# Performance work log

Measured on AMD Instinct MI355X. Metric: run time of the kernel, lower is better.

Reference implementation:

```python
import jax, jax.numpy as jnp
import numpy as np

B, N, TOKEN_DIM = 8, 1024, 768
H, D = 12, 64  # n_heads, head_dim


def setup_inputs() -> dict:
    key = jax.random.key(0)
    k1, k2, k3, k4 = jax.random.split(key, 4)
    x = jax.random.normal(k1, (B, N, TOKEN_DIM), dtype=jnp.float32)
    # nn.Linear(token_dim, 3*H*D, bias=False); store as (in, out)
    W_qkv = jax.random.normal(k2, (TOKEN_DIM, 3 * H * D), dtype=jnp.float32) * (TOKEN_DIM ** -0.5)
    # nn.Linear(H*D, token_dim) with bias
    W_out = jax.random.normal(k3, (H * D, TOKEN_DIM), dtype=jnp.float32) * ((H * D) ** -0.5)
    b_out = jax.random.normal(k4, (TOKEN_DIM,), dtype=jnp.float32) * 0.01
    return {"x": x, "W_qkv": W_qkv, "W_out": W_out, "b_out": b_out}


def reference(x, W_qkv, W_out, b_out):
    b, n, _ = x.shape
    qkv = x @ W_qkv                              # (B, N, 3*H*D)
    # Faithful to original: reshape directly to (B, 3, H, N, D)
    qkv = qkv.reshape(b, 3, H, n, D)
    q, k, v = qkv[:, 0], qkv[:, 1], qkv[:, 2]    # each (B, H, N, D)
    scale = D ** -0.5
    scores = jnp.einsum('bhnd,bhmd->bhnm', q, k) * scale
    probs = jax.nn.softmax(scores, axis=-1)
    attn = jnp.einsum('bhnm,bhmd->bhnd', probs, v)  # (B, H, N, D)
    attn = attn.transpose(0, 2, 1, 3).reshape(b, n, H * D)
    out = attn @ W_out + b_out                    # dropout p=0.0 is identity
    return out
```

## Files before the change

kernel.cpp:

```cpp
#include <hip/hip_runtime.h>
#include <math.h>

static constexpr int NB   = 8;
static constexpr int SEQ  = 1024;
static constexpr int TD   = 768;
static constexpr int NH   = 12;
static constexpr int HD   = 64;
static constexpr int QKVC = 3 * NH * HD;

static constexpr size_t BATCH_ELEMS = (size_t)SEQ * QKVC;
static constexpr size_t THIRD_ELEMS = (size_t)NH * SEQ * HD;
static constexpr size_t HEAD_ELEMS  = (size_t)SEQ * HD;

typedef __bf16 bf16x8 __attribute__((ext_vector_type(8)));
typedef __bf16 bf16x4 __attribute__((ext_vector_type(4)));
typedef float  f32x4  __attribute__((ext_vector_type(4)));

#define MFMA16(a, b, c) __builtin_amdgcn_mfma_f32_16x16x32_bf16((a), (b), (c), 0, 0, 0)

static constexpr float SCL2E = 0.18033688011112042f;

__device__ __forceinline__ void gload_lds16(const void* g, void* l) {
  __builtin_amdgcn_global_load_lds(
      (const __attribute__((address_space(1))) unsigned int*)g,
      (__attribute__((address_space(3))) unsigned int*)l, 16, 0, 0);
}

__global__ __launch_bounds__(256) void cast_f32_bf16(const float* __restrict__ in,
                                                     __bf16* __restrict__ out, int n4) {
  int i = blockIdx.x * 256 + threadIdx.x;
  if (i < n4) {
    float4 v = ((const float4*)in)[i];
    bf16x4 o;
    o[0] = (__bf16)v.x; o[1] = (__bf16)v.y; o[2] = (__bf16)v.z; o[3] = (__bf16)v.w;
    ((bf16x4*)out)[i] = o;
  }
}

__global__ __launch_bounds__(256) void wtrans(const float* __restrict__ W,
                                              __bf16* __restrict__ Wt, int K, int N) {
  __shared__ float T[32 * 33];
  const int tid = threadIdx.x;
  const int k0 = blockIdx.y * 32, n0 = blockIdx.x * 32;
#pragma unroll
  for (int i = 0; i < 4; ++i) {
    int idx = tid + i * 256;
    int kk = idx >> 5, nn = idx & 31;
    T[kk * 33 + nn] = W[(size_t)(k0 + kk) * N + n0 + nn];
  }
  __syncthreads();
#pragma unroll
  for (int i = 0; i < 4; ++i) {
    int idx = tid + i * 256;
    int nn = idx >> 5, kk = idx & 31;
    Wt[(size_t)(n0 + nn) * K + k0 + kk] = (__bf16)T[kk * 33 + nn];
  }
}

__global__ __launch_bounds__(256) void vtrans(const __bf16* __restrict__ qkvb,
                                              __bf16* __restrict__ vtb) {
  const int nt = blockIdx.x;
  const int h = blockIdx.y;
  const int b = blockIdx.z;
  __shared__ __bf16 T[128 * 72];
  const int tid = threadIdx.x;
  const int n0 = nt * 128;
  const __bf16* Vb = qkvb + (size_t)b * BATCH_ELEMS + 2 * THIRD_ELEMS + (size_t)h * HEAD_ELEMS;
#pragma unroll
  for (int i = 0; i < 4; ++i) {
    int ch = tid + i * 256;
    int row = ch >> 3, c8 = ch & 7;
    *(bf16x8*)&T[row * 72 + c8 * 8] = *(const bf16x8*)&Vb[(size_t)(n0 + row) * HD + c8 * 8];
  }
  __syncthreads();
#pragma unroll
  for (int i = 0; i < 4; ++i) {
    int ch = tid + i * 256;
    int d = ch >> 4, n8 = ch & 15;
    bf16x8 v;
#pragma unroll
    for (int j = 0; j < 8; ++j) v[j] = T[(n8 * 8 + j) * 72 + d];
    *(bf16x8*)&vtb[((size_t)((b * NH + h) * HD) + d) * SEQ + n0 + n8 * 8] = v;
  }
}

template <int OUT_BF16>
__global__ __launch_bounds__(256) void gemm_mfma(const __bf16* __restrict__ A,
                                                 const __bf16* __restrict__ Bt,
                                                 const float* __restrict__ bias,
                                                 void* __restrict__ C,
                                                 int M, int N, int K) {
  __shared__ __bf16 As[128 * 32];
  __shared__ __bf16 Bs[128 * 32];
  const int tid = threadIdx.x;
  const int lane = tid & 63;
  const int wid = tid >> 6;
  const int wr = wid >> 1, wc = wid & 1;
  const int r = lane & 15, g = lane >> 4;
  const size_t bm = (size_t)blockIdx.y * 128;
  const size_t bn = (size_t)blockIdx.x * 128;

  const int srow = lane >> 2;
  const int scol = (lane & 3) * 8;

  f32x4 acc[4][4];
#pragma unroll
  for (int mi = 0; mi < 4; ++mi)
#pragma unroll
    for (int nj = 0; nj < 4; ++nj) acc[mi][nj] = (f32x4){0.f, 0.f, 0.f, 0.f};

  for (int k0 = 0; k0 < K; k0 += 32) {
#pragma unroll
    for (int j = 0; j < 2; ++j) {
      const int rowbase = wid * 32 + j * 16;
      gload_lds16(&A[(bm + rowbase + srow) * K + k0 + scol], &As[rowbase * 32]);
      gload_lds16(&Bt[(bn + rowbase + srow) * K + k0 + scol], &Bs[rowbase * 32]);
    }
    __syncthreads();
    bf16x8 af[4], bf[4];
#pragma unroll
    for (int mi = 0; mi < 4; ++mi)
      af[mi] = *(const bf16x8*)&As[(wr * 64 + mi * 16 + r) * 32 + g * 8];
#pragma unroll
    for (int nj = 0; nj < 4; ++nj)
      bf[nj] = *(const bf16x8*)&Bs[(wc * 64 + nj * 16 + r) * 32 + g * 8];
#pragma unroll
    for (int mi = 0; mi < 4; ++mi)
#pragma unroll
      for (int nj = 0; nj < 4; ++nj)
        acc[mi][nj] = MFMA16(af[mi], bf[nj], acc[mi][nj]);
    __syncthreads();
  }

  const int orow0 = g * 4;
  const int ocol = r;
#pragma unroll
  for (int mi = 0; mi < 4; ++mi)
#pragma unroll
    for (int nj = 0; nj < 4; ++nj)
#pragma unroll
      for (int reg = 0; reg < 4; ++reg) {
        size_t rrow = bm + wr * 64 + mi * 16 + orow0 + reg;
        size_t ccol = bn + wc * 64 + nj * 16 + ocol;
        float v = acc[mi][nj][reg];
        if (OUT_BF16)
          ((__bf16*)C)[rrow * N + ccol] = (__bf16)v;
        else
          ((float*)C)[rrow * N + ccol] = v + bias[ccol];
      }
}

__global__ __launch_bounds__(256) void attn_mfma(const __bf16* __restrict__ qkvb,
                                                 const __bf16* __restrict__ vtb,
                                                 __bf16* __restrict__ attn2b) {
  const int d = blockIdx.x;
  const int qt = (d >> 3) & 7;
  const int hb = (d >> 6) * 8 + (d & 7);
  const int b = hb / NH, h = hb % NH;

  const int tid = threadIdx.x;
  const int lane = tid & 63;
  const int w = tid >> 6;
  const int c = lane & 15, g = lane >> 4;

  __shared__ __bf16 KsF[2][4096];
  __shared__ __bf16 VsF[2][4096];

  const __bf16* Qb = qkvb + (size_t)b * BATCH_ELEMS + (size_t)h * HEAD_ELEMS;
  const __bf16* Kb = Qb + THIRD_ELEMS;
  const __bf16* Vtb = vtb + (size_t)((b * NH + h) * HD) * SEQ;

  const __bf16* kS[2];
  const __bf16* vS[2];
  int ldsOff[2];
#pragma unroll
  for (int i = 0; i < 2; ++i) {
    const int t2f = i * 4 + w;
    const int t = t2f >> 1, f = t2f & 1;
    const int krow = ((t >> 1) << 5) | ((c >> 2) << 3) | ((t & 1) << 2) | (c & 3);
    kS[i] = Kb + krow * HD + f * 32 + g * 8;
    const int db = t2f >> 1, kk = t2f & 1;
    vS[i] = Vtb + (db * 16 + c) * SEQ + kk * 32 + g * 8;
    ldsOff[i] = t2f * 512;
  }

  bf16x8 qf[2][2];
#pragma unroll
  for (int s = 0; s < 2; ++s) {
    const int q0s = qt * 128 + s * 64 + w * 16;
#pragma unroll
    for (int f = 0; f < 2; ++f)
      qf[s][f] = *(const bf16x8*)&Qb[(size_t)(q0s + c) * HD + f * 32 + g * 8];
  }

  f32x4 Oa[2][4];
#pragma unroll
  for (int s = 0; s < 2; ++s)
#pragma unroll
    for (int db = 0; db < 4; ++db) Oa[s][db] = (f32x4){0.f, 0.f, 0.f, 0.f};
  float lpart[2] = {0.f, 0.f};

#pragma unroll
  for (int i = 0; i < 2; ++i) {
    gload_lds16(kS[i], &KsF[0][ldsOff[i]]);
    gload_lds16(vS[i], &VsF[0][ldsOff[i]]);
    kS[i] += 64 * HD;
    vS[i] += 64;
  }
  __syncthreads();

  int cur = 0;
  for (int it = 0; it < SEQ / 64; ++it) {
    if (it < SEQ / 64 - 1) {
      const int nxt = cur ^ 1;
#pragma unroll
      for (int i = 0; i < 2; ++i) {
        gload_lds16(kS[i], &KsF[nxt][ldsOff[i]]);
        gload_lds16(vS[i], &VsF[nxt][ldsOff[i]]);
        kS[i] += 64 * HD;
        vS[i] += 64;
      }
    }

    f32x4 sa[2][4];
#pragma unroll
    for (int s = 0; s < 2; ++s)
#pragma unroll
      for (int t = 0; t < 4; ++t) sa[s][t] = (f32x4){0.f, 0.f, 0.f, 0.f};
#pragma unroll
    for (int t = 0; t < 4; ++t)
#pragma unroll
      for (int f = 0; f < 2; ++f) {
        bf16x8 kf = *(const bf16x8*)&KsF[cur][(t * 2 + f) * 512 + lane * 8];
        sa[0][t] = MFMA16(kf, qf[0][f], sa[0][t]);
        sa[1][t] = MFMA16(kf, qf[1][f], sa[1][t]);
      }

    bf16x8 pb[2][2];
#pragma unroll
    for (int s = 0; s < 2; ++s) {
      float p[4][4];
      float lp = 0.f;
#pragma unroll
      for (int t = 0; t < 4; ++t)
#pragma unroll
        for (int reg = 0; reg < 4; ++reg) {
          float pv = __builtin_exp2f(sa[s][t][reg] * SCL2E);
          p[t][reg] = pv;
          lp += pv;
        }
      lpart[s] += lp;
#pragma unroll
      for (int kk = 0; kk < 2; ++kk)
#pragma unroll
        for (int i = 0; i < 4; ++i) {
          pb[s][kk][i] = (__bf16)p[2 * kk][i];
          pb[s][kk][4 + i] = (__bf16)p[2 * kk + 1][i];
        }
    }

#pragma unroll
    for (int db = 0; db < 4; ++db)
#pragma unroll
      for (int kk = 0; kk < 2; ++kk) {
        bf16x8 vf = *(const bf16x8*)&VsF[cur][(db * 2 + kk) * 512 + lane * 8];
        Oa[0][db] = MFMA16(vf, pb[0][kk], Oa[0][db]);
        Oa[1][db] = MFMA16(vf, pb[1][kk], Oa[1][db]);
      }

    __syncthreads();
    cur ^= 1;
  }

#pragma unroll
  for (int s = 0; s < 2; ++s) {
    float lrow = lpart[s];
    lrow += __shfl_xor(lrow, 16);
    lrow += __shfl_xor(lrow, 32);
    const float inv = 1.0f / lrow;
    const size_t rowq = (size_t)(b * SEQ) + qt * 128 + s * 64 + w * 16 + c;
#pragma unroll
    for (int db = 0; db < 4; ++db) {
      bf16x4 o;
#pragma unroll
      for (int reg = 0; reg < 4; ++reg) o[reg] = (__bf16)(Oa[s][db][reg] * inv);
      *(bf16x4*)&attn2b[rowq * TD + h * HD + db * 16 + g * 4] = o;
    }
  }
}

extern "C" void kernel_launch(void* const* d_in, const int* in_sizes, int n_in,
                              void* d_out, int out_size, void* d_ws,
                              size_t ws_size, hipStream_t stream) {
  const float* x = (const float*)d_in[0];
  const float* W_qkv = (const float*)d_in[1];
  const float* W_out = (const float*)d_in[2];
  const float* b_out = (const float*)d_in[3];
  float* out = (float*)d_out;

  __bf16* xb = (__bf16*)d_ws;
  __bf16* wqkvt = xb + (size_t)NB * SEQ * TD;
  __bf16* woutt = wqkvt + (size_t)QKVC * TD;
  __bf16* qkvb = woutt + (size_t)TD * TD;
  __bf16* vtb = qkvb + (size_t)NB * SEQ * QKVC;
  __bf16* attn2b = vtb + (size_t)NB * NH * HD * SEQ;

  cast_f32_bf16<<<(NB * SEQ * TD / 4 + 255) / 256, 256, 0, stream>>>(x, xb, NB * SEQ * TD / 4);
  wtrans<<<dim3(QKVC / 32, TD / 32), 256, 0, stream>>>(W_qkv, wqkvt, TD, QKVC);
  wtrans<<<dim3(TD / 32, TD / 32), 256, 0, stream>>>(W_out, woutt, TD, TD);

  gemm_mfma<1><<<dim3(QKVC / 128, NB * SEQ / 128), 256, 0, stream>>>(
      xb, wqkvt, nullptr, qkvb, NB * SEQ, QKVC, TD);

  vtrans<<<dim3(SEQ / 128, NH, NB), 256, 0, stream>>>(qkvb, vtb);

  attn_mfma<<<dim3(SEQ / 128 * NH * NB), 256, 0, stream>>>(qkvb, vtb, attn2b);

  gemm_mfma<0><<<dim3(TD / 128, NB * SEQ / 128), 256, 0, stream>>>(
      attn2b, woutt, b_out, out, NB * SEQ, TD, TD);
}
```

Baseline: 149.4 us.

## Shrink attention blocks to 2 waves with 32-key tiles and fold scale into Q

The attention kernel now runs 128-thread blocks covering 64 query rows and steps through keys in tiles of 32 instead of 64, which doubles the grid and halves LDS per block for higher occupancy. The softmax scale times log2(e) is folded into the Q third during the QKV GEMM epilogue, which removes a multiply from the inner exp loop. s_setprio is placed around the MFMA sections to favour matrix issue. The trade-off is twice as many loop iterations and barriers per block, and Q is rounded to bf16 after scaling, which slightly changes numerics.

```diff
diff --git a/kernel.cpp b/kernel.cpp
--- a/kernel.cpp
+++ b/kernel.cpp
@@ -84,7 +84,7 @@
   }
 }
 
-template <int OUT_BF16>
+template <int MODE>
 __global__ __launch_bounds__(256) void gemm_mfma(const __bf16* __restrict__ A,
                                                  const __bf16* __restrict__ Bt,
                                                  const float* __restrict__ bias,
@@ -143,19 +143,22 @@
         size_t rrow = bm + wr * 64 + mi * 16 + orow0 + reg;
         size_t ccol = bn + wc * 64 + nj * 16 + ocol;
         float v = acc[mi][nj][reg];
-        if (OUT_BF16)
-          ((__bf16*)C)[rrow * N + ccol] = (__bf16)v;
-        else
+        if (MODE == 1) {
+          int fwb = ((int)(rrow & (SEQ - 1))) * QKVC + (int)ccol;
+          float vv = (fwb < (int)THIRD_ELEMS) ? v * SCL2E : v;
+          ((__bf16*)C)[rrow * N + ccol] = (__bf16)vv;
+        } else {
           ((float*)C)[rrow * N + ccol] = v + bias[ccol];
+        }
       }
 }
 
-__global__ __launch_bounds__(256) void attn_mfma(const __bf16* __restrict__ qkvb,
+__global__ __launch_bounds__(128) void attn_mfma(const __bf16* __restrict__ qkvb,
                                                  const __bf16* __restrict__ vtb,
                                                  __bf16* __restrict__ attn2b) {
   const int d = blockIdx.x;
-  const int qt = (d >> 3) & 7;
-  const int hb = (d >> 6) * 8 + (d & 7);
+  const int qt = (d >> 3) & 15;
+  const int hb = (d >> 7) * 8 + (d & 7);
   const int b = hb / NH, h = hb % NH;
 
   const int tid = threadIdx.x;
@@ -163,8 +166,8 @@
   const int w = tid >> 6;
   const int c = lane & 15, g = lane >> 4;
 
-  __shared__ __bf16 KsF[2][4096];
-  __shared__ __bf16 VsF[2][4096];
+  __shared__ __bf16 KsF[2][2048];
+  __shared__ __bf16 VsF[2][2048];
 
   const __bf16* Qb = qkvb + (size_t)b * BATCH_ELEMS + (size_t)h * HEAD_ELEMS;
   const __bf16* Kb = Qb + THIRD_ELEMS;
@@ -175,19 +178,18 @@
   int ldsOff[2];
 #pragma unroll
   for (int i = 0; i < 2; ++i) {
-    const int t2f = i * 4 + w;
-    const int t = t2f >> 1, f = t2f & 1;
-    const int krow = ((t >> 1) << 5) | ((c >> 2) << 3) | ((t & 1) << 2) | (c & 3);
+    const int grp = i * 2 + w;
+    const int t = grp >> 1, f = grp & 1;
+    const int krow = ((c >> 2) << 3) + (t << 2) + (c & 3);
     kS[i] = Kb + krow * HD + f * 32 + g * 8;
-    const int db = t2f >> 1, kk = t2f & 1;
-    vS[i] = Vtb + (db * 16 + c) * SEQ + kk * 32 + g * 8;
-    ldsOff[i] = t2f * 512;
+    vS[i] = Vtb + (grp * 16 + c) * SEQ + g * 8;
+    ldsOff[i] = grp * 512;
   }
 
   bf16x8 qf[2][2];
 #pragma unroll
   for (int s = 0; s < 2; ++s) {
-    const int q0s = qt * 128 + s * 64 + w * 16;
+    const int q0s = qt * 64 + s * 32 + w * 16;
 #pragma unroll
     for (int f = 0; f < 2; ++f)
       qf[s][f] = *(const bf16x8*)&Qb[(size_t)(q0s + c) * HD + f * 32 + g * 8];
@@ -204,69 +206,63 @@
   for (int i = 0; i < 2; ++i) {
     gload_lds16(kS[i], &KsF[0][ldsOff[i]]);
     gload_lds16(vS[i], &VsF[0][ldsOff[i]]);
-    kS[i] += 64 * HD;
-    vS[i] += 64;
+    kS[i] += 32 * HD;
+    vS[i] += 32;
   }
   __syncthreads();
 
   int cur = 0;
-  for (int it = 0; it < SEQ / 64; ++it) {
-    if (it < SEQ / 64 - 1) {
+  for (int it = 0; it < SEQ / 32; ++it) {
+    if (it < SEQ / 32 - 1) {
       const int nxt = cur ^ 1;
 #pragma unroll
       for (int i = 0; i < 2; ++i) {
         gload_lds16(kS[i], &KsF[nxt][ldsOff[i]]);
         gload_lds16(vS[i], &VsF[nxt][ldsOff[i]]);
-        kS[i] += 64 * HD;
-        vS[i] += 64;
+        kS[i] += 32 * HD;
+        vS[i] += 32;
       }
     }
 
-    f32x4 sa[2][4];
+    f32x4 sa[2][2];
 #pragma unroll
     for (int s = 0; s < 2; ++s)
 #pragma unroll
-      for (int t = 0; t < 4; ++t) sa[s][t] = (f32x4){0.f, 0.f, 0.f, 0.f};
-#pragma unroll
-    for (int t = 0; t < 4; ++t)
+      for (int t = 0; t < 2; ++t) sa[s][t] = (f32x4){0.f, 0.f, 0.f, 0.f};
+    __builtin_amdgcn_s_setprio(1);
+#pragma unroll
+    for (int t = 0; t < 2; ++t)
 #pragma unroll
       for (int f = 0; f < 2; ++f) {
         bf16x8 kf = *(const bf16x8*)&KsF[cur][(t * 2 + f) * 512 + lane * 8];
         sa[0][t] = MFMA16(kf, qf[0][f], sa[0][t]);
         sa[1][t] = MFMA16(kf, qf[1][f], sa[1][t]);
       }
-
-    bf16x8 pb[2][2];
+    __builtin_amdgcn_s_setprio(0);
+
+    bf16x8 pb[2];
 #pragma unroll
     for (int s = 0; s < 2; ++s) {
-      float p[4][4];
       float lp = 0.f;
 #pragma unroll
-      for (int t = 0; t < 4; ++t)
+      for (int t = 0; t < 2; ++t)
 #pragma unroll
         for (int reg = 0; reg < 4; ++reg) {
-          float pv = __builtin_exp2f(sa[s][t][reg] * SCL2E);
-          p[t][reg] = pv;
+          float pv = __builtin_exp2f(sa[s][t][reg]);
+          pb[s][t * 4 + reg] = (__bf16)pv;
           lp += pv;
         }
       lpart[s] += lp;
-#pragma unroll
-      for (int kk = 0; kk < 2; ++kk)
-#pragma unroll
-        for (int i = 0; i < 4; ++i) {
-          pb[s][kk][i] = (__bf16)p[2 * kk][i];
-          pb[s][kk][4 + i] = (__bf16)p[2 * kk + 1][i];
-        }
-    }
-
-#pragma unroll
-    for (int db = 0; db < 4; ++db)
-#pragma unroll
-      for (int kk = 0; kk < 2; ++kk) {
-        bf16x8 vf = *(const bf16x8*)&VsF[cur][(db * 2 + kk) * 512 + lane * 8];
-        Oa[0][db] = MFMA16(vf, pb[0][kk], Oa[0][db]);
-        Oa[1][db] = MFMA16(vf, pb[1][kk], Oa[1][db]);
-      }
+    }
+
+    __builtin_amdgcn_s_setprio(1);
+#pragma unroll
+    for (int db = 0; db < 4; ++db) {
+      bf16x8 vf = *(const bf16x8*)&VsF[cur][db * 512 + lane * 8];
+      Oa[0][db] = MFMA16(vf, pb[0], Oa[0][db]);
+      Oa[1][db] = MFMA16(vf, pb[1], Oa[1][db]);
+    }
+    __builtin_amdgcn_s_setprio(0);
 
     __syncthreads();
     cur ^= 1;
@@ -278,7 +274,7 @@
     lrow += __shfl_xor(lrow, 16);
     lrow += __shfl_xor(lrow, 32);
     const float inv = 1.0f / lrow;
-    const size_t rowq = (size_t)(b * SEQ) + qt * 128 + s * 64 + w * 16 + c;
+    const size_t rowq = (size_t)(b * SEQ) + qt * 64 + s * 32 + w * 16 + c;
 #pragma unroll
     for (int db = 0; db < 4; ++db) {
       bf16x4 o;
@@ -314,7 +310,7 @@
 
   vtrans<<<dim3(SEQ / 128, NH, NB), 256, 0, stream>>>(qkvb, vtb);
 
-  attn_mfma<<<dim3(SEQ / 128 * NH * NB), 256, 0, stream>>>(qkvb, vtb, attn2b);
+  attn_mfma<<<dim3(SEQ / 64 * NH * NB), 128, 0, stream>>>(qkvb, vtb, attn2b);
 
   gemm_mfma<0><<<dim3(TD / 128, NB * SEQ / 128), 256, 0, stream>>>(
       attn2b, woutt, b_out, out, NB * SEQ, TD, TD);
```

Result: slower. 162.4 us (+8.6%).
